# Kernel tuning notes

Hardware: AMD Instinct MI355X
Metric: run time of the kernel (lower is better)

## Reference

```python
import jax, jax.numpy as jnp
import numpy as np

N_NODES = 50000
N_EDGES = 800000


def gcn_layer(x, edge_index, W, b):
    # GCNConv with normalize=False: out[i] = sum_{(j->i) in E} (x_j @ W) + b
    src, dst = edge_index[0], edge_index[1]
    h = x @ W                          # [N, F_out] transform first (cheaper)
    msg = h[src]                       # [E, F_out] gather
    agg = jax.ops.segment_sum(msg, dst, num_segments=x.shape[0])  # scatter-sum
    return agg + b


def setup_inputs() -> dict:
    key = jax.random.key(0)
    ks = jax.random.split(key, 6)
    x = jax.random.normal(ks[0], (N_NODES, 128), dtype=jnp.float32)
    edge_index = jax.random.randint(ks[1], (2, N_EDGES), 0, N_NODES, dtype=jnp.int64)
    # Glorot-ish scaling for stability through 3 layers
    W1 = jax.random.normal(ks[2], (128, 256), dtype=jnp.float32) * (1.0 / np.sqrt(128))
    W2 = jax.random.normal(ks[3], (256, 256), dtype=jnp.float32) * (1.0 / np.sqrt(256))
    W3 = jax.random.normal(ks[4], (256, 256), dtype=jnp.float32) * (1.0 / np.sqrt(256))
    b1 = jnp.zeros((256,), jnp.float32)
    b2 = jnp.zeros((256,), jnp.float32)
    b3 = jnp.zeros((256,), jnp.float32)
    return {"x": x, "edge_index": edge_index, "W1": W1, "b1": b1,
            "W2": W2, "b2": b2, "W3": W3, "b3": b3}


def reference(x, edge_index, W1, b1, W2, b2, W3, b3):
    h = jax.nn.relu(gcn_layer(x, edge_index, W1, b1))
    h = jax.nn.relu(gcn_layer(h, edge_index, W2, b2))
    h = jax.nn.relu(gcn_layer(h, edge_index, W3, b3))
    return h
```

## Files before the change

### kernel.cpp

```cpp
#include <hip/hip_runtime.h>
#include <hip/hip_bf16.h>


#define NBIN 98
#define BINSH 9

typedef short bf16x8 __attribute__((ext_vector_type(8)));
typedef float f32x4 __attribute__((ext_vector_type(4)));

__device__ __forceinline__ short f2bf(float f) {
    __hip_bfloat16 b = __float2bfloat16(f);
    return *reinterpret_cast<short*>(&b);
}
__device__ __forceinline__ float bf2f(short s) {
    union { unsigned u; float f; } c;
    c.u = ((unsigned)(unsigned short)s) << 16;
    return c.f;
}

__global__ void wconvert(const float* __restrict__ W, short* __restrict__ Wt, int K) {
    int idx = blockIdx.x * blockDim.x + threadIdx.x;
    if (idx >= K * 256) return;
    int n = idx / K, k = idx - n * K;
    Wt[idx] = f2bf(W[k * 256 + n]);
}

__global__ void xconvert(const float4* __restrict__ x, short* __restrict__ xb, int n4) {
    int idx = blockIdx.x * blockDim.x + threadIdx.x;
    if (idx >= n4) return;
    float4 v = x[idx];
    short tmp[4] = { f2bf(v.x), f2bf(v.y), f2bf(v.z), f2bf(v.w) };
    *reinterpret_cast<uint2*>(&xb[idx * 4]) = *reinterpret_cast<uint2*>(tmp);
}


__global__ void coarse_hist(const int* __restrict__ ei, int* __restrict__ cbin, int E) {
    __shared__ int h[NBIN];
    for (int i = threadIdx.x; i < NBIN; i += 256) h[i] = 0;
    __syncthreads();
    int base = blockIdx.x * 4096;
#pragma unroll
    for (int i = 0; i < 16; ++i) {
        int e = base + i * 256 + threadIdx.x;
        if (e < E) atomicAdd(&h[ei[E + e] >> BINSH], 1);
    }
    __syncthreads();
    for (int i = threadIdx.x; i < NBIN; i += 256)
        if (h[i]) atomicAdd(&cbin[i], h[i]);
}

__global__ void coarse_scan(const int* __restrict__ cbin, int* __restrict__ cstart,
                            int* __restrict__ gcursor, int E) {
    __shared__ int lds[128];
    int v = (threadIdx.x < NBIN) ? cbin[threadIdx.x] : 0;
    lds[threadIdx.x] = v;
    __syncthreads();
    for (int d = 1; d < 128; d <<= 1) {
        int t = (threadIdx.x >= d) ? lds[threadIdx.x - d] : 0;
        __syncthreads();
        lds[threadIdx.x] += t;
        __syncthreads();
    }
    if (threadIdx.x < NBIN) {
        int ex = lds[threadIdx.x] - v;
        cstart[threadIdx.x] = ex;
        gcursor[threadIdx.x] = ex;
    }
    if (threadIdx.x == 0) cstart[NBIN] = E;
}

__global__ void bin_fill(const int* __restrict__ ei, int* __restrict__ gcursor,
                         unsigned* __restrict__ staging, int E) {
    __shared__ int h[NBIN];
    __shared__ int cur[NBIN];
    for (int i = threadIdx.x; i < NBIN; i += 256) h[i] = 0;
    __syncthreads();
    int base = blockIdx.x * 4096;
    int d_[16], s_[16];
#pragma unroll
    for (int i = 0; i < 16; ++i) {
        int e = base + i * 256 + threadIdx.x;
        if (e < E) {
            s_[i] = ei[e];
            d_[i] = ei[E + e];
            atomicAdd(&h[d_[i] >> BINSH], 1);
        } else d_[i] = -1;
    }
    __syncthreads();
    for (int i = threadIdx.x; i < NBIN; i += 256)
        cur[i] = h[i] ? atomicAdd(&gcursor[i], h[i]) : 0;
    __syncthreads();
#pragma unroll
    for (int i = 0; i < 16; ++i) {
        if (d_[i] >= 0) {
            int p = atomicAdd(&cur[d_[i] >> BINSH], 1);
            staging[p] = ((unsigned)(d_[i] & 511) << 16) | (unsigned)s_[i];
        }
    }
}

__global__ void bin_deg(const unsigned* __restrict__ staging, const int* __restrict__ cstart,
                        int* __restrict__ deg, int N) {
    __shared__ int cnt[512];
    int b = blockIdx.x;
    for (int i = threadIdx.x; i < 512; i += 256) cnt[i] = 0;
    __syncthreads();
    int s = cstart[b], e = cstart[b + 1];
    for (int p = s + threadIdx.x; p < e; p += 256)
        atomicAdd(&cnt[staging[p] >> 16], 1);
    __syncthreads();
    int nb0 = b << BINSH;
    for (int i = threadIdx.x; i < 512; i += 256)
        if (nb0 + i < N) deg[nb0 + i] = cnt[i];
}

__global__ void deg_block_sum(const int* __restrict__ deg, int* __restrict__ bsum, int n) {
    int i = blockIdx.x * 256 + threadIdx.x;
    int v = (i < n) ? deg[i] : 0;
#pragma unroll
    for (int o = 32; o > 0; o >>= 1) v += __shfl_down(v, o, 64);
    __shared__ int wsum[4];
    if ((threadIdx.x & 63) == 0) wsum[threadIdx.x >> 6] = v;
    __syncthreads();
    if (threadIdx.x == 0) bsum[blockIdx.x] = wsum[0] + wsum[1] + wsum[2] + wsum[3];
}

__global__ void scan_bsum(const int* __restrict__ bsum, int* __restrict__ bbase, int nb) {
    __shared__ int lds[256];
    int v = (threadIdx.x < nb) ? bsum[threadIdx.x] : 0;
    lds[threadIdx.x] = v;
    __syncthreads();
    for (int d = 1; d < 256; d <<= 1) {
        int t = (threadIdx.x >= d) ? lds[threadIdx.x - d] : 0;
        __syncthreads();
        lds[threadIdx.x] += t;
        __syncthreads();
    }
    if (threadIdx.x < nb) bbase[threadIdx.x] = lds[threadIdx.x] - v;
}

__global__ void scan_blocks(const int* __restrict__ deg, const int* __restrict__ bbase,
                            int* __restrict__ off, int n) {
    __shared__ int lds[256];
    int i = blockIdx.x * 256 + threadIdx.x;
    int v = (i < n) ? deg[i] : 0;
    lds[threadIdx.x] = v;
    __syncthreads();
    for (int d = 1; d < 256; d <<= 1) {
        int t = (threadIdx.x >= d) ? lds[threadIdx.x - d] : 0;
        __syncthreads();
        lds[threadIdx.x] += t;
        __syncthreads();
    }
    if (i < n) off[i] = lds[threadIdx.x] - v + bbase[blockIdx.x];
}

__global__ void bin_place(const unsigned* __restrict__ staging, const int* __restrict__ cstart,
                          const int* __restrict__ off, int* __restrict__ csr, int N) {
    __shared__ int cur[512];
    int b = blockIdx.x;
    int nb0 = b << BINSH;
    for (int i = threadIdx.x; i < 512; i += 256)
        cur[i] = (nb0 + i < N) ? off[nb0 + i] : 0;
    __syncthreads();
    int s = cstart[b], e = cstart[b + 1];
    for (int p = s + threadIdx.x; p < e; p += 256) {
        unsigned v = staging[p];
        int pos = atomicAdd(&cur[v >> 16], 1);
        csr[pos] = (int)(v & 0xFFFFu);
    }
}


template <int VEC>
__global__ void gather_csr_bf16(const short* __restrict__ h, short* __restrict__ agg,
                                const int* __restrict__ off, const int* __restrict__ deg,
                                const int* __restrict__ csr, int N) {
    typedef short svec __attribute__((ext_vector_type(VEC)));
    const int gw = (blockIdx.x * blockDim.x + threadIdx.x) >> 6;
    if (gw >= N) return;
    const int lane = threadIdx.x & 63;
    const int col = lane * VEC;
    const int F = 64 * VEC;
    const int base = off[gw];
    const int d = deg[gw];

    float acc[VEC];
#pragma unroll
    for (int q = 0; q < VEC; ++q) acc[q] = 0.0f;

    int j = 0;
    for (; j + 4 <= d; j += 4) {
        int s0 = csr[base + j], s1 = csr[base + j + 1];
        int s2 = csr[base + j + 2], s3 = csr[base + j + 3];
        svec v0 = *reinterpret_cast<const svec*>(h + (size_t)s0 * F + col);
        svec v1 = *reinterpret_cast<const svec*>(h + (size_t)s1 * F + col);
        svec v2 = *reinterpret_cast<const svec*>(h + (size_t)s2 * F + col);
        svec v3 = *reinterpret_cast<const svec*>(h + (size_t)s3 * F + col);
#pragma unroll
        for (int q = 0; q < VEC; ++q)
            acc[q] += (bf2f(v0[q]) + bf2f(v1[q])) + (bf2f(v2[q]) + bf2f(v3[q]));
    }
    for (; j < d; ++j) {
        int s = csr[base + j];
        svec v = *reinterpret_cast<const svec*>(h + (size_t)s * F + col);
#pragma unroll
        for (int q = 0; q < VEC; ++q) acc[q] += bf2f(v[q]);
    }
    svec o;
#pragma unroll
    for (int q = 0; q < VEC; ++q) o[q] = f2bf(acc[q]);
    *reinterpret_cast<svec*>(agg + (size_t)gw * F + col) = o;
}


template <typename OutT>
__launch_bounds__(256)
__global__ void gemm_bias_relu(const short* __restrict__ A, const short* __restrict__ Wt,
                               const float* __restrict__ bias, OutT* __restrict__ out,
                               int M, int K) {
    __shared__ short As[128][72];
    __shared__ short Bs[128][72];

    const int tid = threadIdx.x;
    const int lane = tid & 63, wid = tid >> 6;
    const int wr = wid >> 1, wc = wid & 1;
    const int lr = lane & 15, lg = lane >> 4;
    const int m0 = blockIdx.x * 128;
    const int n0 = blockIdx.y * 128;

    f32x4 acc[4][4];
#pragma unroll
    for (int i = 0; i < 4; ++i)
#pragma unroll
        for (int j = 0; j < 4; ++j)
#pragma unroll
            for (int r = 0; r < 4; ++r) acc[i][j][r] = 0.0f;

    const int srow = tid >> 2;
    const int scol = (tid & 3) << 4;

    for (int k0 = 0; k0 < K; k0 += 64) {
        __syncthreads();
#pragma unroll
        for (int pass = 0; pass < 2; ++pass) {
            int row = pass * 64 + srow;
            int gm = m0 + row;
            if (gm < M) {
                const uint4* ap = reinterpret_cast<const uint4*>(A + (size_t)gm * K + k0 + scol);
                *reinterpret_cast<uint4*>(&As[row][scol])     = ap[0];
                *reinterpret_cast<uint4*>(&As[row][scol + 8]) = ap[1];
            } else {
                uint4 z = {0, 0, 0, 0};
                *reinterpret_cast<uint4*>(&As[row][scol])     = z;
                *reinterpret_cast<uint4*>(&As[row][scol + 8]) = z;
            }
            const uint4* bp = reinterpret_cast<const uint4*>(Wt + (size_t)(n0 + row) * K + k0 + scol);
            *reinterpret_cast<uint4*>(&Bs[row][scol])     = bp[0];
            *reinterpret_cast<uint4*>(&Bs[row][scol + 8]) = bp[1];
        }
        __syncthreads();

#pragma unroll
        for (int ksub = 0; ksub < 2; ++ksub) {
            const int kb = ksub * 32 + 4 * lg;
            bf16x8 a[4], b[4];
#pragma unroll
            for (int mi = 0; mi < 4; ++mi) {
                int row = wr * 64 + mi * 16 + lr;
                uint2* pa = reinterpret_cast<uint2*>(&a[mi]);
                pa[0] = *reinterpret_cast<const uint2*>(&As[row][kb]);
                pa[1] = *reinterpret_cast<const uint2*>(&As[row][kb + 16]);
            }
#pragma unroll
            for (int ni = 0; ni < 4; ++ni) {
                int row = wc * 64 + ni * 16 + lr;
                uint2* pb = reinterpret_cast<uint2*>(&b[ni]);
                pb[0] = *reinterpret_cast<const uint2*>(&Bs[row][kb]);
                pb[1] = *reinterpret_cast<const uint2*>(&Bs[row][kb + 16]);
            }
#pragma unroll
            for (int mi = 0; mi < 4; ++mi)
#pragma unroll
                for (int ni = 0; ni < 4; ++ni)
                    acc[mi][ni] = __builtin_amdgcn_mfma_f32_16x16x32_bf16(a[mi], b[ni], acc[mi][ni], 0, 0, 0);
        }
    }

    float bv[4];
#pragma unroll
    for (int ni = 0; ni < 4; ++ni) bv[ni] = bias[n0 + wc * 64 + ni * 16 + lr];
#pragma unroll
    for (int mi = 0; mi < 4; ++mi) {
        int gmBase = m0 + wr * 64 + mi * 16 + 4 * lg;
#pragma unroll
        for (int r = 0; r < 4; ++r) {
            int gm = gmBase + r;
            if (gm >= M) continue;
#pragma unroll
            for (int ni = 0; ni < 4; ++ni) {
                int gn = n0 + wc * 64 + ni * 16 + lr;
                float v = acc[mi][ni][r] + bv[ni];
                v = v > 0.0f ? v : 0.0f;
                if constexpr (sizeof(OutT) == 2)
                    out[(size_t)gm * 256 + gn] = (OutT)f2bf(v);
                else
                    out[(size_t)gm * 256 + gn] = (OutT)v;
            }
        }
    }
}

extern "C" void kernel_launch(void* const* d_in, const int* in_sizes, int n_in,
                              void* d_out, int out_size, void* d_ws, size_t ws_size,
                              hipStream_t stream) {
    const float* x  = (const float*)d_in[0];
    const int*   ei = (const int*)d_in[1];
    const float* W1 = (const float*)d_in[2];
    const float* b1 = (const float*)d_in[3];
    const float* W2 = (const float*)d_in[4];
    const float* b2 = (const float*)d_in[5];
    const float* W3 = (const float*)d_in[6];
    const float* b3 = (const float*)d_in[7];
    float* out = (float*)d_out;
    short* hb  = (short*)d_out;

    const int Nn = 50000, E = 800000, F0 = 128, F = 256;
    const int NB = (Nn + 255) / 256;
    const int EB = (E + 4095) / 4096;

    short* aggb = (short*)d_ws;
    short* xb   = aggb + (size_t)Nn * F;
    short* Wt1  = xb + (size_t)Nn * F0;
    short* Wt2  = Wt1 + F0 * F;
    short* Wt3  = Wt2 + F * F;
    int* deg     = (int*)(Wt3 + F * F);
    int* off     = deg + Nn;
    int* bsum    = off + Nn;
    int* bbase   = bsum + NB;
    int* cbin    = bbase + NB;
    int* cstart  = cbin + NBIN;
    int* gcursor = cstart + NBIN + 1;
    unsigned* staging = (unsigned*)(gcursor + NBIN);
    int* csr     = (int*)(staging + E);

    wconvert<<<(F0 * F + 255) / 256, 256, 0, stream>>>(W1, Wt1, F0);
    wconvert<<<(F * F + 255) / 256, 256, 0, stream>>>(W2, Wt2, F);
    wconvert<<<(F * F + 255) / 256, 256, 0, stream>>>(W3, Wt3, F);
    xconvert<<<(Nn * F0 / 4 + 255) / 256, 256, 0, stream>>>((const float4*)x, xb, Nn * F0 / 4);

    hipMemsetAsync(cbin, 0, NBIN * 4, stream);
    coarse_hist<<<EB, 256, 0, stream>>>(ei, cbin, E);
    coarse_scan<<<1, 128, 0, stream>>>(cbin, cstart, gcursor, E);
    bin_fill<<<EB, 256, 0, stream>>>(ei, gcursor, staging, E);
    bin_deg<<<NBIN, 256, 0, stream>>>(staging, cstart, deg, Nn);
    deg_block_sum<<<NB, 256, 0, stream>>>(deg, bsum, Nn);
    scan_bsum<<<1, 256, 0, stream>>>(bsum, bbase, NB);
    scan_blocks<<<NB, 256, 0, stream>>>(deg, bbase, off, Nn);
    bin_place<<<NBIN, 256, 0, stream>>>(staging, cstart, off, csr, Nn);

    const dim3 gemmGrid((Nn + 127) / 128, 2);
    const int gatherBlocks = (Nn * 64 + 255) / 256;

    gather_csr_bf16<2><<<gatherBlocks, 256, 0, stream>>>(xb, aggb, off, deg, csr, Nn);
    gemm_bias_relu<short><<<gemmGrid, 256, 0, stream>>>(aggb, Wt1, b1, hb, Nn, F0);

    gather_csr_bf16<4><<<gatherBlocks, 256, 0, stream>>>(hb, aggb, off, deg, csr, Nn);
    gemm_bias_relu<short><<<gemmGrid, 256, 0, stream>>>(aggb, Wt2, b2, hb, Nn, F);

    gather_csr_bf16<4><<<gatherBlocks, 256, 0, stream>>>(hb, aggb, off, deg, csr, Nn);
    gemm_bias_relu<float><<<gemmGrid, 256, 0, stream>>>(aggb, Wt3, b3, out, Nn, F);
}
```

Baseline: 302.1 us.

## Fuse prep and CSR build kernels, widen GEMM tile to full output width

Merges the three weight conversions and the x conversion into one launch. It replaces the degree count, three-stage global scan and placement kernels with one per-bin finalize kernel that computes offsets from the bin start plus a local scan. The gather now derives degree from consecutive offsets. The GEMM uses 512-thread blocks covering all 256 output columns, so each A tile is loaded once, at the cost of more LDS per block and half as many blocks.

```diff
diff --git a/kernel.cpp b/kernel.cpp
--- a/kernel.cpp
+++ b/kernel.cpp
@@ -18,19 +18,28 @@
     return c.f;
 }
 
-__global__ void wconvert(const float* __restrict__ W, short* __restrict__ Wt, int K) {
-    int idx = blockIdx.x * blockDim.x + threadIdx.x;
-    if (idx >= K * 256) return;
-    int n = idx / K, k = idx - n * K;
-    Wt[idx] = f2bf(W[k * 256 + n]);
-}
-
-__global__ void xconvert(const float4* __restrict__ x, short* __restrict__ xb, int n4) {
-    int idx = blockIdx.x * blockDim.x + threadIdx.x;
-    if (idx >= n4) return;
-    float4 v = x[idx];
-    short tmp[4] = { f2bf(v.x), f2bf(v.y), f2bf(v.z), f2bf(v.w) };
-    *reinterpret_cast<uint2*>(&xb[idx * 4]) = *reinterpret_cast<uint2*>(tmp);
+__global__ void prep(const float* __restrict__ W1, const float* __restrict__ W2,
+                     const float* __restrict__ W3, const float4* __restrict__ x,
+                     short* __restrict__ Wt1, short* __restrict__ Wt2,
+                     short* __restrict__ Wt3, short* __restrict__ xb) {
+    int idx = blockIdx.x * 256 + threadIdx.x;
+    if (idx < 32768) {
+        int n = idx >> 7, k = idx & 127;
+        Wt1[idx] = f2bf(W1[k * 256 + n]);
+    } else if (idx < 98304) {
+        int i = idx - 32768, n = i >> 8, k = i & 255;
+        Wt2[i] = f2bf(W2[k * 256 + n]);
+    } else if (idx < 163840) {
+        int i = idx - 98304, n = i >> 8, k = i & 255;
+        Wt3[i] = f2bf(W3[k * 256 + n]);
+    } else {
+        int i = idx - 163840;
+        if (i < 1600000) {
+            float4 v = x[i];
+            short tmp[4] = { f2bf(v.x), f2bf(v.y), f2bf(v.z), f2bf(v.w) };
+            *reinterpret_cast<uint2*>(&xb[i * 4]) = *reinterpret_cast<uint2*>(tmp);
+        }
+    }
 }
 
 
@@ -50,7 +59,8 @@
 }
 
 __global__ void coarse_scan(const int* __restrict__ cbin, int* __restrict__ cstart,
-                            int* __restrict__ gcursor, int E) {
+                            int* __restrict__ gcursor, int* __restrict__ off,
+                            int E, int N) {
     __shared__ int lds[128];
     int v = (threadIdx.x < NBIN) ? cbin[threadIdx.x] : 0;
     lds[threadIdx.x] = v;
@@ -66,7 +76,7 @@
         cstart[threadIdx.x] = ex;
         gcursor[threadIdx.x] = ex;
     }
-    if (threadIdx.x == 0) cstart[NBIN] = E;
+    if (threadIdx.x == 0) { cstart[NBIN] = E; off[N] = E; }
 }
 
 __global__ void bin_fill(const int* __restrict__ ei, int* __restrict__ gcursor,
@@ -99,72 +109,35 @@
     }
 }
 
-__global__ void bin_deg(const unsigned* __restrict__ staging, const int* __restrict__ cstart,
-                        int* __restrict__ deg, int N) {
+__global__ void bin_finalize(const unsigned* __restrict__ staging,
+                             const int* __restrict__ cstart,
+                             int* __restrict__ off, int* __restrict__ csr, int N) {
     __shared__ int cnt[512];
-    int b = blockIdx.x;
-    for (int i = threadIdx.x; i < 512; i += 256) cnt[i] = 0;
-    __syncthreads();
-    int s = cstart[b], e = cstart[b + 1];
-    for (int p = s + threadIdx.x; p < e; p += 256)
-        atomicAdd(&cnt[staging[p] >> 16], 1);
-    __syncthreads();
+    __shared__ int psum[256];
+    __shared__ int cur[512];
+    const int b = blockIdx.x, t = threadIdx.x;
+    cnt[t] = 0; cnt[t + 256] = 0;
+    __syncthreads();
+    const int s = cstart[b], e = cstart[b + 1];
+    for (int p = s + t; p < e; p += 256) atomicAdd(&cnt[staging[p] >> 16], 1);
+    __syncthreads();
+    int c0 = cnt[2 * t], c1 = cnt[2 * t + 1];
+    psum[t] = c0 + c1;
+    __syncthreads();
+    for (int d = 1; d < 256; d <<= 1) {
+        int v = (t >= d) ? psum[t - d] : 0;
+        __syncthreads();
+        psum[t] += v;
+        __syncthreads();
+    }
+    int base = s + (t ? psum[t - 1] : 0);
     int nb0 = b << BINSH;
-    for (int i = threadIdx.x; i < 512; i += 256)
-        if (nb0 + i < N) deg[nb0 + i] = cnt[i];
-}
-
-__global__ void deg_block_sum(const int* __restrict__ deg, int* __restrict__ bsum, int n) {
-    int i = blockIdx.x * 256 + threadIdx.x;
-    int v = (i < n) ? deg[i] : 0;
-#pragma unroll
-    for (int o = 32; o > 0; o >>= 1) v += __shfl_down(v, o, 64);
-    __shared__ int wsum[4];
-    if ((threadIdx.x & 63) == 0) wsum[threadIdx.x >> 6] = v;
-    __syncthreads();
-    if (threadIdx.x == 0) bsum[blockIdx.x] = wsum[0] + wsum[1] + wsum[2] + wsum[3];
-}
-
-__global__ void scan_bsum(const int* __restrict__ bsum, int* __restrict__ bbase, int nb) {
-    __shared__ int lds[256];
-    int v = (threadIdx.x < nb) ? bsum[threadIdx.x] : 0;
-    lds[threadIdx.x] = v;
-    __syncthreads();
-    for (int d = 1; d < 256; d <<= 1) {
-        int t = (threadIdx.x >= d) ? lds[threadIdx.x - d] : 0;
-        __syncthreads();
-        lds[threadIdx.x] += t;
-        __syncthreads();
-    }
-    if (threadIdx.x < nb) bbase[threadIdx.x] = lds[threadIdx.x] - v;
-}
-
-__global__ void scan_blocks(const int* __restrict__ deg, const int* __restrict__ bbase,
-                            int* __restrict__ off, int n) {
-    __shared__ int lds[256];
-    int i = blockIdx.x * 256 + threadIdx.x;
-    int v = (i < n) ? deg[i] : 0;
-    lds[threadIdx.x] = v;
-    __syncthreads();
-    for (int d = 1; d < 256; d <<= 1) {
-        int t = (threadIdx.x >= d) ? lds[threadIdx.x - d] : 0;
-        __syncthreads();
-        lds[threadIdx.x] += t;
-        __syncthreads();
-    }
-    if (i < n) off[i] = lds[threadIdx.x] - v + bbase[blockIdx.x];
-}
-
-__global__ void bin_place(const unsigned* __restrict__ staging, const int* __restrict__ cstart,
-                          const int* __restrict__ off, int* __restrict__ csr, int N) {
-    __shared__ int cur[512];
-    int b = blockIdx.x;
-    int nb0 = b << BINSH;
-    for (int i = threadIdx.x; i < 512; i += 256)
-        cur[i] = (nb0 + i < N) ? off[nb0 + i] : 0;
-    __syncthreads();
-    int s = cstart[b], e = cstart[b + 1];
-    for (int p = s + threadIdx.x; p < e; p += 256) {
+    cur[2 * t] = base;
+    cur[2 * t + 1] = base + c0;
+    if (nb0 + 2 * t < N)     off[nb0 + 2 * t]     = base;
+    if (nb0 + 2 * t + 1 < N) off[nb0 + 2 * t + 1] = base + c0;
+    __syncthreads();
+    for (int p = s + t; p < e; p += 256) {
         unsigned v = staging[p];
         int pos = atomicAdd(&cur[v >> 16], 1);
         csr[pos] = (int)(v & 0xFFFFu);
@@ -174,8 +147,8 @@
 
 template <int VEC>
 __global__ void gather_csr_bf16(const short* __restrict__ h, short* __restrict__ agg,
-                                const int* __restrict__ off, const int* __restrict__ deg,
-                                const int* __restrict__ csr, int N) {
+                                const int* __restrict__ off, const int* __restrict__ csr,
+                                int N) {
     typedef short svec __attribute__((ext_vector_type(VEC)));
     const int gw = (blockIdx.x * blockDim.x + threadIdx.x) >> 6;
     if (gw >= N) return;
@@ -183,7 +156,7 @@
     const int col = lane * VEC;
     const int F = 64 * VEC;
     const int base = off[gw];
-    const int d = deg[gw];
+    const int d = off[gw + 1] - base;
 
     float acc[VEC];
 #pragma unroll
@@ -215,19 +188,18 @@
 
 
 template <typename OutT>
-__launch_bounds__(256)
+__launch_bounds__(512)
 __global__ void gemm_bias_relu(const short* __restrict__ A, const short* __restrict__ Wt,
                                const float* __restrict__ bias, OutT* __restrict__ out,
                                int M, int K) {
     __shared__ short As[128][72];
-    __shared__ short Bs[128][72];
+    __shared__ short Bs[256][72];
 
     const int tid = threadIdx.x;
     const int lane = tid & 63, wid = tid >> 6;
-    const int wr = wid >> 1, wc = wid & 1;
+    const int wr = wid >> 2, wc = wid & 3;
     const int lr = lane & 15, lg = lane >> 4;
     const int m0 = blockIdx.x * 128;
-    const int n0 = blockIdx.y * 128;
 
     f32x4 acc[4][4];
 #pragma unroll
@@ -237,27 +209,29 @@
 #pragma unroll
             for (int r = 0; r < 4; ++r) acc[i][j][r] = 0.0f;
 
-    const int srow = tid >> 2;
-    const int scol = (tid & 3) << 4;
+    const int srA = tid >> 2;
+    const int scA = (tid & 3) << 4;
+    const int srB = tid >> 1;
+    const int scB = (tid & 1) << 5;
 
     for (int k0 = 0; k0 < K; k0 += 64) {
         __syncthreads();
-#pragma unroll
-        for (int pass = 0; pass < 2; ++pass) {
-            int row = pass * 64 + srow;
-            int gm = m0 + row;
+        {
+            int gm = m0 + srA;
             if (gm < M) {
-                const uint4* ap = reinterpret_cast<const uint4*>(A + (size_t)gm * K + k0 + scol);
-                *reinterpret_cast<uint4*>(&As[row][scol])     = ap[0];
-                *reinterpret_cast<uint4*>(&As[row][scol + 8]) = ap[1];
+                const uint4* ap = reinterpret_cast<const uint4*>(A + (size_t)gm * K + k0 + scA);
+                *reinterpret_cast<uint4*>(&As[srA][scA])     = ap[0];
+                *reinterpret_cast<uint4*>(&As[srA][scA + 8]) = ap[1];
             } else {
                 uint4 z = {0, 0, 0, 0};
-                *reinterpret_cast<uint4*>(&As[row][scol])     = z;
-                *reinterpret_cast<uint4*>(&As[row][scol + 8]) = z;
+                *reinterpret_cast<uint4*>(&As[srA][scA])     = z;
+                *reinterpret_cast<uint4*>(&As[srA][scA + 8]) = z;
             }
-            const uint4* bp = reinterpret_cast<const uint4*>(Wt + (size_t)(n0 + row) * K + k0 + scol);
-            *reinterpret_cast<uint4*>(&Bs[row][scol])     = bp[0];
-            *reinterpret_cast<uint4*>(&Bs[row][scol + 8]) = bp[1];
+            const uint4* bp = reinterpret_cast<const uint4*>(Wt + (size_t)srB * K + k0 + scB);
+            *reinterpret_cast<uint4*>(&Bs[srB][scB])      = bp[0];
+            *reinterpret_cast<uint4*>(&Bs[srB][scB + 8])  = bp[1];
+            *reinterpret_cast<uint4*>(&Bs[srB][scB + 16]) = bp[2];
+            *reinterpret_cast<uint4*>(&Bs[srB][scB + 24]) = bp[3];
         }
         __syncthreads();
 
@@ -289,7 +263,7 @@
 
     float bv[4];
 #pragma unroll
-    for (int ni = 0; ni < 4; ++ni) bv[ni] = bias[n0 + wc * 64 + ni * 16 + lr];
+    for (int ni = 0; ni < 4; ++ni) bv[ni] = bias[wc * 64 + ni * 16 + lr];
 #pragma unroll
     for (int mi = 0; mi < 4; ++mi) {
         int gmBase = m0 + wr * 64 + mi * 16 + 4 * lg;
@@ -299,7 +273,7 @@
             if (gm >= M) continue;
 #pragma unroll
             for (int ni = 0; ni < 4; ++ni) {
-                int gn = n0 + wc * 64 + ni * 16 + lr;
+                int gn = wc * 64 + ni * 16 + lr;
                 float v = acc[mi][ni][r] + bv[ni];
                 v = v > 0.0f ? v : 0.0f;
                 if constexpr (sizeof(OutT) == 2)
@@ -326,7 +300,6 @@
     short* hb  = (short*)d_out;
 
     const int Nn = 50000, E = 800000, F0 = 128, F = 256;
-    const int NB = (Nn + 255) / 256;
     const int EB = (E + 4095) / 4096;
 
     short* aggb = (short*)d_ws;
@@ -334,40 +307,31 @@
     short* Wt1  = xb + (size_t)Nn * F0;
     short* Wt2  = Wt1 + F0 * F;
     short* Wt3  = Wt2 + F * F;
-    int* deg     = (int*)(Wt3 + F * F);
-    int* off     = deg + Nn;
-    int* bsum    = off + Nn;
-    int* bbase   = bsum + NB;
-    int* cbin    = bbase + NB;
+    int* off     = (int*)(Wt3 + F * F);
+    int* cbin    = off + Nn + 1;
     int* cstart  = cbin + NBIN;
     int* gcursor = cstart + NBIN + 1;
     unsigned* staging = (unsigned*)(gcursor + NBIN);
     int* csr     = (int*)(staging + E);
 
-    wconvert<<<(F0 * F + 255) / 256, 256, 0, stream>>>(W1, Wt1, F0);
-    wconvert<<<(F * F + 255) / 256, 256, 0, stream>>>(W2, Wt2, F);
-    wconvert<<<(F * F + 255) / 256, 256, 0, stream>>>(W3, Wt3, F);
-    xconvert<<<(Nn * F0 / 4 + 255) / 256, 256, 0, stream>>>((const float4*)x, xb, Nn * F0 / 4);
+    prep<<<(163840 + 1600000 + 255) / 256, 256, 0, stream>>>(
+        W1, W2, W3, (const float4*)x, Wt1, Wt2, Wt3, xb);
 
     hipMemsetAsync(cbin, 0, NBIN * 4, stream);
     coarse_hist<<<EB, 256, 0, stream>>>(ei, cbin, E);
-    coarse_scan<<<1, 128, 0, stream>>>(cbin, cstart, gcursor, E);
+    coarse_scan<<<1, 128, 0, stream>>>(cbin, cstart, gcursor, off, E, Nn);
     bin_fill<<<EB, 256, 0, stream>>>(ei, gcursor, staging, E);
-    bin_deg<<<NBIN, 256, 0, stream>>>(staging, cstart, deg, Nn);
-    deg_block_sum<<<NB, 256, 0, stream>>>(deg, bsum, Nn);
-    scan_bsum<<<1, 256, 0, stream>>>(bsum, bbase, NB);
-    scan_blocks<<<NB, 256, 0, stream>>>(deg, bbase, off, Nn);
-    bin_place<<<NBIN, 256, 0, stream>>>(staging, cstart, off, csr, Nn);
-
-    const dim3 gemmGrid((Nn + 127) / 128, 2);
+    bin_finalize<<<NBIN, 256, 0, stream>>>(staging, cstart, off, csr, Nn);
+
+    const int gemmGrid = (Nn + 127) / 128;
     const int gatherBlocks = (Nn * 64 + 255) / 256;
 
-    gather_csr_bf16<2><<<gatherBlocks, 256, 0, stream>>>(xb, aggb, off, deg, csr, Nn);
-    gemm_bias_relu<short><<<gemmGrid, 256, 0, stream>>>(aggb, Wt1, b1, hb, Nn, F0);
-
-    gather_csr_bf16<4><<<gatherBlocks, 256, 0, stream>>>(hb, aggb, off, deg, csr, Nn);
-    gemm_bias_relu<short><<<gemmGrid, 256, 0, stream>>>(aggb, Wt2, b2, hb, Nn, F);
-
-    gather_csr_bf16<4><<<gatherBlocks, 256, 0, stream>>>(hb, aggb, off, deg, csr, Nn);
-    gemm_bias_relu<float><<<gemmGrid, 256, 0, stream>>>(aggb, Wt3, b3, out, Nn, F);
-}
+    gather_csr_bf16<2><<<gatherBlocks, 256, 0, stream>>>(xb, aggb, off, csr, Nn);
+    gemm_bias_relu<short><<<gemmGrid, 512, 0, stream>>>(aggb, Wt1, b1, hb, Nn, F0);
+
+    gather_csr_bf16<4><<<gatherBlocks, 256, 0, stream>>>(hb, aggb, off, csr, Nn);
+    gemm_bias_relu<short><<<gemmGrid, 512, 0, stream>>>(aggb, Wt2, b2, hb, Nn, F);
+
+    gather_csr_bf16<4><<<gatherBlocks, 256, 0, stream>>>(hb, aggb, off, csr, Nn);
+    gemm_bias_relu<float><<<gemmGrid, 512, 0, stream>>>(aggb, Wt3, b3, out, Nn, F);
+}
```

Result: faster. 264.9 us (-12.3%).
